# Kernel tuning notes

Measured on AMD Instinct MI355X. Metric: run time of the kernel, lower is better.

The kernel has to match this reference:

```python
import jax, jax.numpy as jnp
import numpy as np

N_NODES = 20000
N_EDGES = 640000
D = 64        # node / edge feature dim
H = 128       # MLP hidden dim


def setup_inputs() -> dict:
    key = jax.random.key(0)
    ks = jax.random.split(key, 12)
    inp = {
        "x": jax.random.normal(ks[0], (N_NODES, D), dtype=jnp.float32),
        "edge_index": jax.random.randint(ks[1], (2, N_EDGES), 0, N_NODES, dtype=jnp.int64),
        "edge_attr": jax.random.normal(ks[2], (N_EDGES, D), dtype=jnp.float32),
        "f": jax.random.normal(ks[3], (N_NODES, D), dtype=jnp.float32),
        # edge MLP: concat(x_src, x_dest, edge_attr) = 3D -> H -> D
        "We1": jax.random.normal(ks[4], (3 * D, H), dtype=jnp.float32) / np.sqrt(3 * D),
        "be1": jnp.zeros((H,), dtype=jnp.float32),
        "We2": jax.random.normal(ks[5], (H, D), dtype=jnp.float32) / np.sqrt(H),
        "be2": jnp.zeros((D,), dtype=jnp.float32),
        # node MLP: concat(x, agg, f) = 3D -> H -> D
        "Wn1": jax.random.normal(ks[6], (3 * D, H), dtype=jnp.float32) / np.sqrt(3 * D),
        "bn1": jnp.zeros((H,), dtype=jnp.float32),
        "Wn2": jax.random.normal(ks[7], (H, D), dtype=jnp.float32) / np.sqrt(H),
        "bn2": jnp.zeros((D,), dtype=jnp.float32),
    }
    return inp


def reference(x, edge_index, edge_attr, f, We1, be1, We2, be2, Wn1, bn1, Wn2, bn2):
    src, dest = edge_index[0], edge_index[1]
    # edge model: MLP over gathered src/dest node features + edge attrs
    e_in = jnp.concatenate([x[src], x[dest], edge_attr], axis=-1)      # [E, 3D]
    e_h = jax.nn.relu(e_in @ We1 + be1)                                 # [E, H]
    edge_out = e_h @ We2 + be2                                          # [E, D]
    # node model: scatter-add edge messages to dest, then MLP
    agg = jax.ops.segment_sum(edge_out, dest, num_segments=N_NODES)    # [N, D]
    n_in = jnp.concatenate([x, agg, f], axis=-1)                        # [N, 3D]
    n_h = jax.nn.relu(n_in @ Wn1 + bn1)                                 # [N, H]
    x_out = n_h @ Wn2 + bn2                                             # [N, D]
    return (x_out, edge_out)
```

## Files before the change

### kernel.cpp

```cpp
#include <hip/hip_runtime.h>

#define NE 640000
#define NN 20000
#define SEI 200
#define SEH 136
#define SEO 68

typedef __attribute__((ext_vector_type(8))) short s16x8;
typedef __attribute__((ext_vector_type(4))) short s16x4;
typedef __attribute__((ext_vector_type(4))) float f32x4;

typedef const __attribute__((ext_vector_type(4))) float cf32x4;

__device__ __forceinline__ short f2bf(float f) {
  unsigned int u = __float_as_uint(f);
  u += 0x7fffu + ((u >> 16) & 1u);
  return (short)(u >> 16);
}

__device__ __forceinline__ s16x8 cvt8(f32x4 a, f32x4 b) {
  s16x8 o;
  o[0]=f2bf(a[0]); o[1]=f2bf(a[1]); o[2]=f2bf(a[2]); o[3]=f2bf(a[3]);
  o[4]=f2bf(b[0]); o[5]=f2bf(b[1]); o[6]=f2bf(b[2]); o[7]=f2bf(b[3]);
  return o;
}

__device__ __forceinline__ void load_wfrags_lds(const float* W1, const float* W2,
                                                const float* b1, const float* b2,
                                                short* smem, int t,
                                                int wv, int r, int g,
                                                s16x8 w1f[2][6], s16x8 w2f[4],
                                                f32x4 b1r[2], f32x4* b2r) {
  #pragma unroll
  for (int i = 0; i < 24; ++i) {
    int idx4 = t + i * 256;
    f32x4 v = ((cf32x4*)W1)[idx4];
    s16x4 pk; pk[0]=f2bf(v[0]); pk[1]=f2bf(v[1]); pk[2]=f2bf(v[2]); pk[3]=f2bf(v[3]);
    *(s16x4*)&smem[idx4 * 4] = pk;
  }
  __syncthreads();
  #pragma unroll
  for (int nn = 0; nn < 2; ++nn) {
    const int h = (wv*2+nn)*16 + r;
    #pragma unroll
    for (int kk = 0; kk < 6; ++kk) {
      s16x8 wf;
      #pragma unroll
      for (int i = 0; i < 8; ++i) wf[i] = smem[(kk*32 + g*8 + i)*128 + h];
      w1f[nn][kk] = wf;
    }
    b1r[nn] = *(cf32x4*)(b1 + (wv*2+nn)*16 + g*4);
  }
  __syncthreads();
  #pragma unroll
  for (int i = 0; i < 8; ++i) {
    int idx4 = t + i * 256;
    f32x4 v = ((cf32x4*)W2)[idx4];
    s16x4 pk; pk[0]=f2bf(v[0]); pk[1]=f2bf(v[1]); pk[2]=f2bf(v[2]); pk[3]=f2bf(v[3]);
    *(s16x4*)&smem[idx4 * 4] = pk;
  }
  __syncthreads();
  {
    const int h2 = wv*16 + r;
    #pragma unroll
    for (int kk = 0; kk < 4; ++kk) {
      s16x8 wf;
      #pragma unroll
      for (int i = 0; i < 8; ++i) wf[i] = smem[(kk*32 + g*8 + i)*64 + h2];
      w2f[kk] = wf;
    }
    *b2r = *(cf32x4*)(b2 + wv*16 + g*4);
  }
  __syncthreads();
}


__global__ void count_kernel(const int* __restrict__ eidx, int* __restrict__ cursor) {
  const int4* d4 = (const int4*)(eidx + NE);
  int i = blockIdx.x * blockDim.x + threadIdx.x;
  if (i < NE / 4) {
    int4 d = d4[i];
    atomicAdd(&cursor[d.x], 1);
    atomicAdd(&cursor[d.y], 1);
    atomicAdd(&cursor[d.z], 1);
    atomicAdd(&cursor[d.w], 1);
  }
}

__global__ __launch_bounds__(1024)
void scan_kernel(int* __restrict__ cursor, int* __restrict__ offs) {
  __shared__ int cnt[20480];
  __shared__ int part[1024];
  const int t = threadIdx.x;
  for (int i = t; i < 20480; i += 1024)
    cnt[i] = (i < NN) ? cursor[i] : 0;
  __syncthreads();
  const int lo = t * 20;
  int s = 0;
  #pragma unroll
  for (int k = 0; k < 20; ++k) s += cnt[lo + k];
  part[t] = s;
  __syncthreads();
  for (int d = 1; d < 1024; d <<= 1) {
    int u = (t >= d) ? part[t - d] : 0;
    __syncthreads();
    part[t] += u;
    __syncthreads();
  }
  int run = part[t] - s;
  #pragma unroll
  for (int k = 0; k < 20; ++k) {
    int c = cnt[lo + k];
    cnt[lo + k] = run;
    run += c;
  }
  __syncthreads();
  for (int i = t; i < NN; i += 1024) {
    int v = cnt[i];
    offs[i] = v;
    cursor[i] = v;
  }
  if (t == 1023) offs[NN] = NE;
}

__global__ void scatter_kernel(const int* __restrict__ eidx,
                               int* __restrict__ cursor, int* __restrict__ elist) {
  const int4* d4 = (const int4*)(eidx + NE);
  int i = blockIdx.x * blockDim.x + threadIdx.x;
  if (i < NE / 4) {
    int4 d = d4[i];
    const int e = i * 4;
    elist[atomicAdd(&cursor[d.x], 1)] = e;
    elist[atomicAdd(&cursor[d.y], 1)] = e + 1;
    elist[atomicAdd(&cursor[d.z], 1)] = e + 2;
    elist[atomicAdd(&cursor[d.w], 1)] = e + 3;
  }
}

#define LOAD_ROWS(sv, dv, ee) do {                                        \
    cf32x4* ps_ = (cf32x4*)(x  + (size_t)(sv)*64 + p*16);                 \
    cf32x4* pd_ = (cf32x4*)(x  + (size_t)(dv)*64 + p*16);                 \
    cf32x4* pe_ = (cf32x4*)(ea + (size_t)(ee)*64 + p*16);                 \
    L[0]=ps_[0]; L[1]=ps_[1]; L[2]=ps_[2];  L[3]=ps_[3];                  \
    L[4]=pd_[0]; L[5]=pd_[1]; L[6]=pd_[2];  L[7]=pd_[3];                  \
    L[8]=pe_[0]; L[9]=pe_[1]; L[10]=pe_[2]; L[11]=pe_[3];                 \
  } while (0)

#define WRITE_EIN(buf) do {                                               \
    short* stg_ = (buf) + el*SEI + p*16;                                  \
    ((s16x8*)stg_)[0]       = cvt8(L[0], L[1]);                           \
    ((s16x8*)stg_)[1]       = cvt8(L[2], L[3]);                           \
    ((s16x8*)(stg_+64))[0]  = cvt8(L[4], L[5]);                           \
    ((s16x8*)(stg_+64))[1]  = cvt8(L[6], L[7]);                           \
    ((s16x8*)(stg_+128))[0] = cvt8(L[8], L[9]);                           \
    ((s16x8*)(stg_+128))[1] = cvt8(L[10], L[11]);                         \
  } while (0)

__global__ __launch_bounds__(256, 2)
void edge_kernel(const float* __restrict__ x, const int* __restrict__ eidx,
                 const float* __restrict__ ea, const int* __restrict__ elist,
                 const float* __restrict__ We1, const float* __restrict__ be1,
                 const float* __restrict__ We2, const float* __restrict__ be2,
                 float* __restrict__ edge_out, float* __restrict__ agg)
{
  __shared__ __align__(16) char smem[69632];
  short* sEin0 = (short*)smem;
  short* sEin1 = (short*)(smem + 25600);
  short* sEh   = (short*)(smem + 51200);
  int* sDest0  = (int*)(smem + 68608);
  int* sDest1  = (int*)(smem + 68864);
  int* sEid0   = (int*)(smem + 69120);
  int* sEid1   = (int*)(smem + 69376);

  const int t = threadIdx.x;
  const int wv = t >> 6, lane = t & 63;
  const int r = lane & 15, g = lane >> 4;

  s16x8 w1f[2][6], w2f[4];
  f32x4 b1r[2], b2r;
  load_wfrags_lds(We1, We2, be1, be2, (short*)smem, t, wv, r, g,
                  w1f, w2f, b1r, &b2r);

  const int el = t >> 2, p = t & 3;
  const int nT = NE / 64;
  const int S = (int)gridDim.x;
  const f32x4 zero = {0.f, 0.f, 0.f, 0.f};

  f32x4 L[12];
  int eW = 0, dW = 0;
  int eI = 0, sI = 0, dI = 0;
  int tile = blockIdx.x;

  if (tile < nT) {
    int e0 = elist[(tile << 6) + el];
    int s0 = eidx[e0], d0 = eidx[NE + e0];
    LOAD_ROWS(s0, d0, e0);
    WRITE_EIN(sEin0);
    if (p == 0) { sDest0[el] = d0; sEid0[el] = e0; }
    const int t1 = tile + S;
    if (t1 < nT) {
      eW = elist[(t1 << 6) + el];
      int sv = eidx[eW]; dW = eidx[NE + eW];
      LOAD_ROWS(sv, dW, eW);
    }
    const int t2 = tile + 2 * S;
    if (t2 < nT) {
      eI = elist[(t2 << 6) + el];
      sI = eidx[eI]; dI = eidx[NE + eI];
    }
  }
  __syncthreads();

  int cur = 0;
  while (tile < nT) {
    const short* Ecur = cur ? sEin1 : sEin0;
    short* Enxt = cur ? sEin0 : sEin1;
    float* EoutC = (float*)(cur ? (smem + 25600) : smem);
    const int* sDestC = cur ? sDest1 : sDest0;
    const int* sEidC  = cur ? sEid1  : sEid0;
    int* sDestN = cur ? sDest0 : sDest1;
    int* sEidN  = cur ? sEid0  : sEid1;

    const int tW = tile + S, tI = tile + 2 * S, tX = tile + 3 * S;
    if (tW < nT) {
      WRITE_EIN(Enxt);
      if (p == 0) { sDestN[el] = dW; sEidN[el] = eW; }
    }
    if (tI < nT) { LOAD_ROWS(sI, dI, eI); eW = eI; dW = dI; }
    if (tX < nT) {
      eI = elist[(tX << 6) + el];
      sI = eidx[eI]; dI = eidx[NE + eI];
    }

    f32x4 acc1[2][4];
    #pragma unroll
    for (int nn = 0; nn < 2; ++nn)
      #pragma unroll
      for (int j = 0; j < 4; ++j) acc1[nn][j] = zero;
    #pragma unroll
    for (int kk = 0; kk < 6; ++kk) {
      #pragma unroll
      for (int j = 0; j < 4; ++j) {
        s16x8 ef = *(const s16x8*)&Ecur[(j*16 + r)*SEI + kk*32 + g*8];
        acc1[0][j] = __builtin_amdgcn_mfma_f32_16x16x32_bf16(w1f[0][kk], ef, acc1[0][j], 0, 0, 0);
        acc1[1][j] = __builtin_amdgcn_mfma_f32_16x16x32_bf16(w1f[1][kk], ef, acc1[1][j], 0, 0, 0);
      }
    }
    #pragma unroll
    for (int nn = 0; nn < 2; ++nn)
      #pragma unroll
      for (int j = 0; j < 4; ++j) {
        s16x4 pk;
        #pragma unroll
        for (int q = 0; q < 4; ++q) {
          float v = acc1[nn][j][q] + b1r[nn][q];
          pk[q] = f2bf(v > 0.f ? v : 0.f);
        }
        *(s16x4*)&sEh[(j*16 + r)*SEH + (wv*2+nn)*16 + g*4] = pk;
      }
    __syncthreads();

    #pragma unroll
    for (int j = 0; j < 4; ++j) {
      f32x4 a2 = zero;
      #pragma unroll
      for (int kk = 0; kk < 4; ++kk) {
        s16x8 hf = *(const s16x8*)&sEh[(j*16 + r)*SEH + kk*32 + g*8];
        a2 = __builtin_amdgcn_mfma_f32_16x16x32_bf16(w2f[kk], hf, a2, 0, 0, 0);
      }
      a2 += b2r;
      const int eg = sEidC[j*16 + r];
      *(f32x4*)&edge_out[(size_t)eg*64 + wv*16 + g*4] = a2;
      *(f32x4*)&EoutC[(j*16 + r)*SEO + wv*16 + g*4] = a2;
    }
    __syncthreads();

    {
      const int row0 = wv * 16;
      float acc = EoutC[row0*SEO + lane];
      int dcur = sDestC[row0];
      #pragma unroll
      for (int k = 1; k < 16; ++k) {
        const int dn = sDestC[row0 + k];
        const float v = EoutC[(row0 + k)*SEO + lane];
        if (dn != dcur) {
          unsafeAtomicAdd(&agg[(size_t)dcur*64 + lane], acc);
          acc = v; dcur = dn;
        } else {
          acc += v;
        }
      }
      unsafeAtomicAdd(&agg[(size_t)dcur*64 + lane], acc);
    }
    __syncthreads();
    cur ^= 1;
    tile += S;
  }
}

__global__ __launch_bounds__(256, 2)
void node_kernel(const float* __restrict__ x, const float* agg,
                 const float* __restrict__ f,
                 const float* __restrict__ Wn1, const float* __restrict__ bn1,
                 const float* __restrict__ Wn2, const float* __restrict__ bn2,
                 float* x_out)
{
  __shared__ __align__(16) char smem[49152];
  short* sEin = (short*)smem;
  short* sEh  = (short*)(smem + 25600);

  const int t = threadIdx.x;
  const int wv = t >> 6, lane = t & 63;
  const int r = lane & 15, g = lane >> 4;

  s16x8 w1f[2][6], w2f[4];
  f32x4 b1r[2], b2r;
  load_wfrags_lds(Wn1, Wn2, bn1, bn2, (short*)smem, t, wv, r, g,
                  w1f, w2f, b1r, &b2r);

  const int el = t >> 2, p = t & 3;
  const f32x4 zero = {0.f, 0.f, 0.f, 0.f};
  const int nT = (NN + 63) / 64;

  for (int tile = blockIdx.x; tile < nT; tile += (int)gridDim.x) {
    const int base = tile << 6;
    const int i = base + el;

    f32x4 L[12];
    if (i < NN) {
      cf32x4* ps_ = (cf32x4*)(x   + (size_t)i*64 + p*16);
      cf32x4* pa_ = (cf32x4*)(agg + (size_t)i*64 + p*16);
      cf32x4* pf_ = (cf32x4*)(f   + (size_t)i*64 + p*16);
      L[0]=ps_[0]; L[1]=ps_[1]; L[2]=ps_[2];  L[3]=ps_[3];
      L[4]=pa_[0]; L[5]=pa_[1]; L[6]=pa_[2];  L[7]=pa_[3];
      L[8]=pf_[0]; L[9]=pf_[1]; L[10]=pf_[2]; L[11]=pf_[3];
    } else {
      #pragma unroll
      for (int q = 0; q < 12; ++q) L[q] = zero;
    }
    WRITE_EIN(sEin);
    __syncthreads();

    f32x4 acc1[2][4];
    #pragma unroll
    for (int nn = 0; nn < 2; ++nn)
      #pragma unroll
      for (int j = 0; j < 4; ++j) acc1[nn][j] = zero;
    #pragma unroll
    for (int kk = 0; kk < 6; ++kk) {
      #pragma unroll
      for (int j = 0; j < 4; ++j) {
        s16x8 ef = *(const s16x8*)&sEin[(j*16 + r)*SEI + kk*32 + g*8];
        acc1[0][j] = __builtin_amdgcn_mfma_f32_16x16x32_bf16(w1f[0][kk], ef, acc1[0][j], 0, 0, 0);
        acc1[1][j] = __builtin_amdgcn_mfma_f32_16x16x32_bf16(w1f[1][kk], ef, acc1[1][j], 0, 0, 0);
      }
    }
    #pragma unroll
    for (int nn = 0; nn < 2; ++nn)
      #pragma unroll
      for (int j = 0; j < 4; ++j) {
        s16x4 pk;
        #pragma unroll
        for (int q = 0; q < 4; ++q) {
          float v = acc1[nn][j][q] + b1r[nn][q];
          pk[q] = f2bf(v > 0.f ? v : 0.f);
        }
        *(s16x4*)&sEh[(j*16 + r)*SEH + (wv*2+nn)*16 + g*4] = pk;
      }
    __syncthreads();

    #pragma unroll
    for (int j = 0; j < 4; ++j) {
      f32x4 a2 = zero;
      #pragma unroll
      for (int kk = 0; kk < 4; ++kk) {
        s16x8 hf = *(const s16x8*)&sEh[(j*16 + r)*SEH + kk*32 + g*8];
        a2 = __builtin_amdgcn_mfma_f32_16x16x32_bf16(w2f[kk], hf, a2, 0, 0, 0);
      }
      const int row = base + j*16 + r;
      if (row < NN) {
        f32x4 v = a2 + b2r;
        *(f32x4*)&x_out[(size_t)row*64 + wv*16 + g*4] = v;
      }
    }
  }
}

extern "C" void kernel_launch(void* const* d_in, const int* in_sizes, int n_in,
                              void* d_out, int out_size, void* d_ws, size_t ws_size,
                              hipStream_t stream) {
  const float* x   = (const float*)d_in[0];
  const int*   ei  = (const int*)d_in[1];
  const float* ea  = (const float*)d_in[2];
  const float* f   = (const float*)d_in[3];
  const float* We1 = (const float*)d_in[4];
  const float* be1 = (const float*)d_in[5];
  const float* We2 = (const float*)d_in[6];
  const float* be2 = (const float*)d_in[7];
  const float* Wn1 = (const float*)d_in[8];
  const float* bn1 = (const float*)d_in[9];
  const float* Wn2 = (const float*)d_in[10];
  const float* bn2 = (const float*)d_in[11];

  float* x_out    = (float*)d_out;
  float* edge_out = x_out + (size_t)NN * 64;

  int* cursor = (int*)d_ws;
  int* offs   = cursor + NN;
  int* elist  = offs + NN + 8;

  hipMemsetAsync(x_out, 0, (size_t)NN * 64 * sizeof(float), stream);
  hipMemsetAsync(cursor, 0, NN * sizeof(int), stream);
  count_kernel<<<625, 256, 0, stream>>>(ei, cursor);
  scan_kernel<<<1, 1024, 0, stream>>>(cursor, offs);
  scatter_kernel<<<625, 256, 0, stream>>>(ei, cursor, elist);
  edge_kernel<<<512, 256, 0, stream>>>(x, ei, ea, elist, We1, be1, We2, be2,
                                       edge_out, x_out);
  node_kernel<<<105, 256, 0, stream>>>(x, x_out, f, Wn1, bn1, Wn2, bn2, x_out);
}
```

Before: 227.1 us.

## Assign contiguous tile ranges per block and use lighter LDS-only barriers

The edge kernel now gives each block a contiguous range of 19 or 20 tiles, hardcoded for a fixed grid size, where before it strode by gridDim. Each __syncthreads is replaced by an lgkmcnt wait plus s_barrier, so global stores are no longer waited on, and the trailing barrier per iteration is dropped. The Eout LDS stride changes from 68 to 100, presumably to reduce bank conflicts. Contiguous tiles may improve locality of the sorted edge list and reduce atomic contention. The hardcoded split assumes a specific grid size, and removing the final barrier relies on the double-buffer alternation to stay race-free.

Result: no change. 227.4 us (+0.1%).

```diff
diff --git a/kernel.cpp b/kernel.cpp
--- a/kernel.cpp
+++ b/kernel.cpp
@@ -4,13 +4,19 @@
 #define NN 20000
 #define SEI 200
 #define SEH 136
-#define SEO 68
+#define SEO 100
 
 typedef __attribute__((ext_vector_type(8))) short s16x8;
 typedef __attribute__((ext_vector_type(4))) short s16x4;
 typedef __attribute__((ext_vector_type(4))) float f32x4;
 
 typedef const __attribute__((ext_vector_type(4))) float cf32x4;
+
+#define BARRIER_LGKM() do {                                   \
+    asm volatile("s_waitcnt lgkmcnt(0)" ::: "memory");        \
+    __builtin_amdgcn_s_barrier();                             \
+    __builtin_amdgcn_sched_barrier(0);                        \
+  } while (0)
 
 __device__ __forceinline__ short f2bf(float f) {
   unsigned int u = __float_as_uint(f);
@@ -182,37 +188,37 @@
                   w1f, w2f, b1r, &b2r);
 
   const int el = t >> 2, p = t & 3;
-  const int nT = NE / 64;
-  const int S = (int)gridDim.x;
   const f32x4 zero = {0.f, 0.f, 0.f, 0.f};
+
+  const int b = blockIdx.x;
+  const int t0 = b * 19 + (b < 272 ? b : 272);
+  const int t1 = t0 + (b < 272 ? 20 : 19);
 
   f32x4 L[12];
   int eW = 0, dW = 0;
   int eI = 0, sI = 0, dI = 0;
-  int tile = blockIdx.x;
-
-  if (tile < nT) {
+  int tile = t0;
+
+  {
     int e0 = elist[(tile << 6) + el];
     int s0 = eidx[e0], d0 = eidx[NE + e0];
     LOAD_ROWS(s0, d0, e0);
     WRITE_EIN(sEin0);
     if (p == 0) { sDest0[el] = d0; sEid0[el] = e0; }
-    const int t1 = tile + S;
-    if (t1 < nT) {
-      eW = elist[(t1 << 6) + el];
+    if (tile + 1 < t1) {
+      eW = elist[((tile + 1) << 6) + el];
       int sv = eidx[eW]; dW = eidx[NE + eW];
       LOAD_ROWS(sv, dW, eW);
     }
-    const int t2 = tile + 2 * S;
-    if (t2 < nT) {
-      eI = elist[(t2 << 6) + el];
+    if (tile + 2 < t1) {
+      eI = elist[((tile + 2) << 6) + el];
       sI = eidx[eI]; dI = eidx[NE + eI];
     }
   }
-  __syncthreads();
+  BARRIER_LGKM();
 
   int cur = 0;
-  while (tile < nT) {
+  while (tile < t1) {
     const short* Ecur = cur ? sEin1 : sEin0;
     short* Enxt = cur ? sEin0 : sEin1;
     float* EoutC = (float*)(cur ? (smem + 25600) : smem);
@@ -221,13 +227,13 @@
     int* sDestN = cur ? sDest0 : sDest1;
     int* sEidN  = cur ? sEid0  : sEid1;
 
-    const int tW = tile + S, tI = tile + 2 * S, tX = tile + 3 * S;
-    if (tW < nT) {
+    const int tW = tile + 1, tI = tile + 2, tX = tile + 3;
+    if (tW < t1) {
       WRITE_EIN(Enxt);
       if (p == 0) { sDestN[el] = dW; sEidN[el] = eW; }
     }
-    if (tI < nT) { LOAD_ROWS(sI, dI, eI); eW = eI; dW = dI; }
-    if (tX < nT) {
+    if (tI < t1) { LOAD_ROWS(sI, dI, eI); eW = eI; dW = dI; }
+    if (tX < t1) {
       eI = elist[(tX << 6) + el];
       sI = eidx[eI]; dI = eidx[NE + eI];
     }
@@ -258,7 +264,7 @@
         }
         *(s16x4*)&sEh[(j*16 + r)*SEH + (wv*2+nn)*16 + g*4] = pk;
       }
-    __syncthreads();
+    BARRIER_LGKM();
 
     #pragma unroll
     for (int j = 0; j < 4; ++j) {
@@ -273,7 +279,7 @@
       *(f32x4*)&edge_out[(size_t)eg*64 + wv*16 + g*4] = a2;
       *(f32x4*)&EoutC[(j*16 + r)*SEO + wv*16 + g*4] = a2;
     }
-    __syncthreads();
+    BARRIER_LGKM();
 
     {
       const int row0 = wv * 16;
@@ -292,9 +298,8 @@
       }
       unsafeAtomicAdd(&agg[(size_t)dcur*64 + lane], acc);
     }
-    __syncthreads();
     cur ^= 1;
-    tile += S;
+    tile = tW;
   }
 }
 
```
